# Performance work log

Hardware: AMD Instinct MI355X
Metric: run time of the kernel (lower is better)

## Reference

```python
import jax, jax.numpy as jnp
from jax import lax
import numpy as np

DIM = 768
NUM_TOKENS = 32
B, T, H, W = 16, 1, 32, 32


def setup_inputs() -> dict:
    key = jax.random.key(0)
    ks = jax.random.split(key, 10)
    return {
        "x": jax.random.normal(ks[0], (B, DIM, T, H, W), dtype=jnp.float32),
        "pos": jax.random.normal(ks[1], (B, DIM, T, H, W), dtype=jnp.float32),
        "bn_weight": jax.random.uniform(ks[2], (DIM,), dtype=jnp.float32, minval=0.5, maxval=1.5),
        "bn_bias": jax.random.normal(ks[3], (DIM,), dtype=jnp.float32) * 0.1,
        "bn_mean": jax.random.normal(ks[4], (DIM,), dtype=jnp.float32) * 0.1,
        "bn_var": jax.random.uniform(ks[5], (DIM,), dtype=jnp.float32, minval=0.5, maxval=1.5),
        "dw_weight": jax.random.normal(ks[6], (DIM, 1, 3, 3), dtype=jnp.float32) * 0.1,
        "dw_bias": jax.random.normal(ks[7], (DIM,), dtype=jnp.float32) * 0.1,
        "pw_weight": jax.random.normal(ks[8], (NUM_TOKENS, DIM, 1, 1), dtype=jnp.float32) * 0.05,
        "pw_bias": jax.random.normal(ks[9], (NUM_TOKENS,), dtype=jnp.float32) * 0.1,
    }


def _hardswish(x):
    return x * jnp.clip(x + 3.0, 0.0, 6.0) * (1.0 / 6.0)


def reference(x, pos, bn_weight, bn_bias, bn_mean, bn_var,
              dw_weight, dw_bias, pw_weight, pw_bias):
    eps = 1e-5
    f = x[:, :, 0]  # [B, C, H, W]
    # BatchNorm2d (inference form with running stats)
    scale = bn_weight * lax.rsqrt(bn_var + eps)          # [C]
    shift = bn_bias - bn_mean * scale                    # [C]
    f = f * scale[None, :, None, None] + shift[None, :, None, None]
    # depthwise 3x3 conv (groups = C)
    h = lax.conv_general_dilated(
        f, dw_weight, window_strides=(1, 1), padding="SAME",
        feature_group_count=DIM,
        dimension_numbers=("NCHW", "OIHW", "NCHW"))
    h = h + dw_bias[None, :, None, None]
    h = _hardswish(h)
    # pointwise 1x1 conv -> num_tokens channels
    s = lax.conv_general_dilated(
        h, pw_weight, window_strides=(1, 1), padding="SAME",
        dimension_numbers=("NCHW", "OIHW", "NCHW"))
    s = s + pw_bias[None, :, None, None]                 # [B, Nt, H, W]
    b, nt, hh, ww = s.shape
    st = s.reshape(b, nt, hh * ww)                       # [B, Nt, HW]
    # hard-argmax mask over spatial dim (ties -> multiple ones, as in torch)
    mask = (st == jnp.max(st, axis=2, keepdims=True)).astype(st.dtype)
    feat = f.reshape(b, DIM, hh * ww).transpose(0, 2, 1)  # [B, HW, C]
    result = mask @ feat                                  # [B, Nt, C]
    p = pos[:, :, 0].reshape(b, DIM, hh * ww).transpose(0, 2, 1)
    p = mask @ p                                          # [B, Nt, C]
    return result, p, mask
```

## Files before the change

kernel.cpp:

```cpp
#include <hip/hip_runtime.h>
#include <math.h>

#define DIMC 768
#define BATCH 16
#define HWSZ 1024
#define NT 32
#define SCH 16
#define CHPB 48

#define OUT_P_OFF    393216
#define OUT_MASK_OFF 786432

#define WS_WT_OFF 8388608

__global__ __launch_bounds__(256) void k0_transpose(
    const float* __restrict__ pww, float* __restrict__ wt)
{
    int i = blockIdx.x * 256 + threadIdx.x;
    wt[i] = pww[(i & 31) * DIMC + (i >> 5)];
}


#define ACC4(G) float a##G##0 = 0.f, a##G##1 = 0.f, a##G##2 = 0.f, a##G##3 = 0.f;
#define PW4(G, W) { a##G##0 = fmaf(hs, W.x, a##G##0); a##G##1 = fmaf(hs, W.y, a##G##1); \
                    a##G##2 = fmaf(hs, W.z, a##G##2); a##G##3 = fmaf(hs, W.w, a##G##3); }
#define STG4(G) { po[(size_t)(4*G+0) << 10] = a##G##0; po[(size_t)(4*G+1) << 10] = a##G##1; \
                  po[(size_t)(4*G+2) << 10] = a##G##2; po[(size_t)(4*G+3) << 10] = a##G##3; }

__global__ __launch_bounds__(256) void kf_fused(
    const float* __restrict__ x,
    const float* __restrict__ bnw, const float* __restrict__ bnb,
    const float* __restrict__ bnm, const float* __restrict__ bnv,
    const float* __restrict__ dww, const float* __restrict__ dwb,
    const float* __restrict__ wt,
    float* __restrict__ partials)
{
    const int b   = blockIdx.z;
    const int scc = blockIdx.y;
    const int cb0 = scc * CHPB;
    const int r0  = blockIdx.x * 8;
    const int tid = threadIdx.x;
    const int rl  = tid >> 5;
    const int col = tid & 31;

    __shared__ float st[2][340];
    float* S0 = &st[0][0];
    for (int i = tid; i < 680; i += 256) S0[i] = 0.0f;

    const int i1t = tid + 256;
    const int sr0 = tid / 34, sc0 = tid - sr0 * 34;
    const int sr1 = i1t / 34, sc1 = i1t - sr1 * 34;
    const int rr0 = r0 - 1 + sr0, cl0 = sc0 - 1;
    const int rr1 = r0 - 1 + sr1, cl1 = sc1 - 1;
    const bool valid0 = (rr0 >= 0 && rr0 < 32 && cl0 >= 0 && cl0 < 32);
    const bool valid1 = (i1t < 340) && (rr1 >= 0 && rr1 < 32 && cl1 >= 0 && cl1 < 32);
    const int off0 = rr0 * 32 + cl0;
    const int off1 = rr1 * 32 + cl1;

    const float* xb = x + (size_t)(b * DIMC) * HWSZ;

    {
        const int c = cb0;
        float scale = bnw[c] * rsqrtf(bnv[c] + 1e-5f);
        float shift = bnb[c] - bnm[c] * scale;
        const float* xc = xb + (size_t)c * HWSZ;
        if (valid0) st[0][tid] = xc[off0] * scale + shift;
        if (valid1) st[0][i1t] = xc[off1] * scale + shift;
    }
    __syncthreads();

    ACC4(0) ACC4(1) ACC4(2) ACC4(3) ACC4(4) ACC4(5) ACC4(6) ACC4(7)

    const int base = rl * 34 + col;

    for (int k = 0; k < CHPB; ++k) {
        const int c = cb0 + k;
        const float* S = st[k & 1];

        float g0 = 0.f, g1 = 0.f, scale = 0.f, shift = 0.f;
        if (k < CHPB - 1) {
            const int cn = c + 1;
            scale = bnw[cn] * rsqrtf(bnv[cn] + 1e-5f);
            shift = bnb[cn] - bnm[cn] * scale;
            const float* xc = xb + (size_t)cn * HWSZ;
            if (valid0) g0 = xc[off0];
            if (valid1) g1 = xc[off1];
        }

        const float* wd = dww + c * 9;
        float racc = dwb[c];
        racc = fmaf(wd[0], S[base +  0], racc);
        racc = fmaf(wd[1], S[base +  1], racc);
        racc = fmaf(wd[2], S[base +  2], racc);
        racc = fmaf(wd[3], S[base + 34], racc);
        racc = fmaf(wd[4], S[base + 35], racc);
        racc = fmaf(wd[5], S[base + 36], racc);
        racc = fmaf(wd[6], S[base + 68], racc);
        racc = fmaf(wd[7], S[base + 69], racc);
        racc = fmaf(wd[8], S[base + 70], racc);
        float clp = fminf(fmaxf(racc + 3.0f, 0.0f), 6.0f);
        float hs  = racc * clp * (1.0f / 6.0f);

        const float4* wv = (const float4*)(wt + c * NT);
        float4 wA = wv[0], wB = wv[1], wC = wv[2], wD = wv[3],
               wE = wv[4], wF = wv[5], wG = wv[6], wH = wv[7];
        PW4(0, wA) PW4(1, wB) PW4(2, wC) PW4(3, wD)
        PW4(4, wE) PW4(5, wF) PW4(6, wG) PW4(7, wH)

        if (k < CHPB - 1) {
            float* Sn = &st[(k & 1) ^ 1][0];
            if (valid0) Sn[tid] = fmaf(g0, scale, shift);
            if (valid1) Sn[i1t] = fmaf(g1, scale, shift);
        }
        __syncthreads();
    }

    float* po = partials + ((size_t)(scc * BATCH + b) * NT) * HWSZ
              + blockIdx.x * 256 + tid;
    STG4(0) STG4(1) STG4(2) STG4(3) STG4(4) STG4(5) STG4(6) STG4(7)
}

__global__ __launch_bounds__(256) void k3_mask_gather(
    const float* __restrict__ partials,
    const float* __restrict__ x, const float* __restrict__ posin,
    const float* __restrict__ bnw, const float* __restrict__ bnb,
    const float* __restrict__ bnm, const float* __restrict__ bnv,
    float* __restrict__ out)
{
    int bt = blockIdx.x;
    int b  = bt >> 5;
    int t  = bt & 31;
    int tid = threadIdx.x;

    const float* pp = partials + ((size_t)(b * NT) + t) * HWSZ;
    float v[4];
    float m = -INFINITY;
#pragma unroll
    for (int i = 0; i < 4; ++i) {
        int pos = tid + 256 * i;
        float acc = 0.0f;
#pragma unroll
        for (int s = 0; s < SCH; ++s)
            acc += pp[(size_t)s * (BATCH * NT * HWSZ) + pos];
        v[i] = acc;
        m = fmaxf(m, acc);
    }
#pragma unroll
    for (int off = 32; off; off >>= 1)
        m = fmaxf(m, __shfl_xor(m, off));
    __shared__ float wm[4];
    if ((tid & 63) == 0) wm[tid >> 6] = m;
    __syncthreads();
    m = fmaxf(fmaxf(wm[0], wm[1]), fmaxf(wm[2], wm[3]));

    __shared__ int nmatch;
    __shared__ int matchpos[16];
    if (tid == 0) nmatch = 0;
    __syncthreads();

    float* maskp = out + OUT_MASK_OFF + (size_t)bt * HWSZ;
#pragma unroll
    for (int i = 0; i < 4; ++i) {
        int pos = tid + 256 * i;
        int hit = (v[i] == m);
        maskp[pos] = hit ? 1.0f : 0.0f;
        if (hit) {
            int k = atomicAdd(&nmatch, 1);
            if (k < 16) matchpos[k] = pos;
        }
    }
    __syncthreads();
    int nm = nmatch < 16 ? nmatch : 16;

    const float* xb = x + (size_t)b * DIMC * HWSZ;
    const float* pb = posin + (size_t)b * DIMC * HWSZ;
    for (int c = tid; c < DIMC; c += 256) {
        float scale = bnw[c] * rsqrtf(bnv[c] + 1e-5f);
        float shift = bnb[c] - bnm[c] * scale;
        float rf = 0.0f, rp = 0.0f;
        for (int k = 0; k < nm; ++k) {
            int pos = matchpos[k];
            rf += xb[(size_t)c * HWSZ + pos] * scale + shift;
            rp += pb[(size_t)c * HWSZ + pos];
        }
        out[(size_t)bt * DIMC + c] = rf;
        out[OUT_P_OFF + (size_t)bt * DIMC + c] = rp;
    }
}

extern "C" void kernel_launch(void* const* d_in, const int* in_sizes, int n_in,
                              void* d_out, int out_size, void* d_ws, size_t ws_size,
                              hipStream_t stream)
{
    const float* x    = (const float*)d_in[0];
    const float* pos  = (const float*)d_in[1];
    const float* bnw  = (const float*)d_in[2];
    const float* bnb  = (const float*)d_in[3];
    const float* bnm  = (const float*)d_in[4];
    const float* bnv  = (const float*)d_in[5];
    const float* dww  = (const float*)d_in[6];
    const float* dwb  = (const float*)d_in[7];
    const float* pww  = (const float*)d_in[8];
    float* out = (float*)d_out;

    float* partials = (float*)d_ws;
    float* wt       = (float*)d_ws + WS_WT_OFF;

    k0_transpose<<<96, 256, 0, stream>>>(pww, wt);
    kf_fused<<<dim3(4, SCH, BATCH), 256, 0, stream>>>(x, bnw, bnb, bnm, bnv,
                                                      dww, dwb, wt, partials);
    k3_mask_gather<<<BATCH * NT, 256, 0, stream>>>(partials, x, pos,
                                                   bnw, bnb, bnm, bnv, out);
}
```

Before: 66.83 us.

## Stage four channels per barrier in fused conv and vectorize mask reduction

The fused depthwise+pointwise kernel now loads and normalizes four input channels per shared-memory stage instead of one. This cuts the number of __syncthreads from 48 to 12 per block and gives each thread more independent global loads in flight. The mask-gather kernel reads the split-K partials and writes the mask with float4 accesses instead of strided scalars. The cost is more shared memory and registers (six prefetch slots plus select logic), which may lower occupancy.

```diff
diff --git a/kernel.cpp b/kernel.cpp
--- a/kernel.cpp
+++ b/kernel.cpp
@@ -7,6 +7,8 @@
 #define NT 32
 #define SCH 16
 #define CHPB 48
+#define CPM 4
+#define NMAC 12
 
 #define OUT_P_OFF    393216
 #define OUT_MASK_OFF 786432
@@ -26,6 +28,35 @@
                     a##G##2 = fmaf(hs, W.z, a##G##2); a##G##3 = fmaf(hs, W.w, a##G##3); }
 #define STG4(G) { po[(size_t)(4*G+0) << 10] = a##G##0; po[(size_t)(4*G+1) << 10] = a##G##1; \
                   po[(size_t)(4*G+2) << 10] = a##G##2; po[(size_t)(4*G+3) << 10] = a##G##3; }
+
+#define CONV_PW(Q) { \
+    const int c = cm + Q; \
+    const float* wd = dww + c * 9; \
+    float r = dwb[c]; \
+    const float* S = Sc + (Q) * 340 + base; \
+    r = fmaf(wd[0], S[0],  r); \
+    r = fmaf(wd[1], S[1],  r); \
+    r = fmaf(wd[2], S[2],  r); \
+    r = fmaf(wd[3], S[34], r); \
+    r = fmaf(wd[4], S[35], r); \
+    r = fmaf(wd[5], S[36], r); \
+    r = fmaf(wd[6], S[68], r); \
+    r = fmaf(wd[7], S[69], r); \
+    r = fmaf(wd[8], S[70], r); \
+    float clp = fminf(fmaxf(r + 3.0f, 0.0f), 6.0f); \
+    float hs  = r * clp * (1.0f / 6.0f); \
+    const float4* wv = (const float4*)(wt + c * NT); \
+    float4 wA = wv[0], wB = wv[1], wC = wv[2], wD = wv[3], \
+           wE = wv[4], wF = wv[5], wG = wv[6], wH = wv[7]; \
+    PW4(0, wA) PW4(1, wB) PW4(2, wC) PW4(3, wD) \
+    PW4(4, wE) PW4(5, wF) PW4(6, wG) PW4(7, wH) }
+
+__device__ __forceinline__ float sel4(int cu, float v0, float v1, float v2, float v3)
+{
+    float a = (cu & 1) ? v1 : v0;
+    float b = (cu & 1) ? v3 : v2;
+    return (cu & 2) ? b : a;
+}
 
 __global__ __launch_bounds__(256) void kf_fused(
     const float* __restrict__ x,
@@ -43,29 +74,42 @@
     const int rl  = tid >> 5;
     const int col = tid & 31;
 
-    __shared__ float st[2][340];
-    float* S0 = &st[0][0];
-    for (int i = tid; i < 680; i += 256) S0[i] = 0.0f;
-
-    const int i1t = tid + 256;
-    const int sr0 = tid / 34, sc0 = tid - sr0 * 34;
-    const int sr1 = i1t / 34, sc1 = i1t - sr1 * 34;
-    const int rr0 = r0 - 1 + sr0, cl0 = sc0 - 1;
-    const int rr1 = r0 - 1 + sr1, cl1 = sc1 - 1;
-    const bool valid0 = (rr0 >= 0 && rr0 < 32 && cl0 >= 0 && cl0 < 32);
-    const bool valid1 = (i1t < 340) && (rr1 >= 0 && rr1 < 32 && cl1 >= 0 && cl1 < 32);
-    const int off0 = rr0 * 32 + cl0;
-    const int off1 = rr1 * 32 + cl1;
+    __shared__ float st[2][CPM * 340];
+
+    for (int i = tid; i < 2 * CPM * 340; i += 256) ((float*)st)[i] = 0.0f;
+
+    int  soff[6]; bool svalid[6]; int scu[6];
+#pragma unroll
+    for (int u = 0; u < 6; ++u) {
+        int idx = tid + 256 * u;
+        int cu  = idx / 340;
+        int rem = idx - cu * 340;
+        int sr  = rem / 34, sc = rem - sr * 34;
+        int rr  = r0 - 1 + sr, cc = sc - 1;
+        svalid[u] = (idx < CPM * 340) && rr >= 0 && rr < 32 && cc >= 0 && cc < 32;
+        scu[u]  = cu;
+        soff[u] = cu * HWSZ + rr * 32 + cc;
+    }
 
     const float* xb = x + (size_t)(b * DIMC) * HWSZ;
 
     {
-        const int c = cb0;
-        float scale = bnw[c] * rsqrtf(bnv[c] + 1e-5f);
-        float shift = bnb[c] - bnm[c] * scale;
-        const float* xc = xb + (size_t)c * HWSZ;
-        if (valid0) st[0][tid] = xc[off0] * scale + shift;
-        if (valid1) st[0][i1t] = xc[off1] * scale + shift;
+        const int cm = cb0;
+        float g[6];
+#pragma unroll
+        for (int u = 0; u < 6; ++u)
+            g[u] = svalid[u] ? xb[(size_t)cm * HWSZ + soff[u]] : 0.0f;
+        float s0 = bnw[cm+0] * rsqrtf(bnv[cm+0] + 1e-5f), h0 = bnb[cm+0] - bnm[cm+0] * s0;
+        float s1 = bnw[cm+1] * rsqrtf(bnv[cm+1] + 1e-5f), h1 = bnb[cm+1] - bnm[cm+1] * s1;
+        float s2 = bnw[cm+2] * rsqrtf(bnv[cm+2] + 1e-5f), h2 = bnb[cm+2] - bnm[cm+2] * s2;
+        float s3 = bnw[cm+3] * rsqrtf(bnv[cm+3] + 1e-5f), h3 = bnb[cm+3] - bnm[cm+3] * s3;
+        float* Sn = &st[0][0];
+#pragma unroll
+        for (int u = 0; u < 6; ++u) {
+            float scl = sel4(scu[u], s0, s1, s2, s3);
+            float shf = sel4(scu[u], h0, h1, h2, h3);
+            if (svalid[u]) Sn[tid + 256 * u] = fmaf(g[u], scl, shf);
+        }
     }
     __syncthreads();
 
@@ -73,44 +117,33 @@
 
     const int base = rl * 34 + col;
 
-    for (int k = 0; k < CHPB; ++k) {
-        const int c = cb0 + k;
-        const float* S = st[k & 1];
-
-        float g0 = 0.f, g1 = 0.f, scale = 0.f, shift = 0.f;
-        if (k < CHPB - 1) {
-            const int cn = c + 1;
-            scale = bnw[cn] * rsqrtf(bnv[cn] + 1e-5f);
-            shift = bnb[cn] - bnm[cn] * scale;
-            const float* xc = xb + (size_t)cn * HWSZ;
-            if (valid0) g0 = xc[off0];
-            if (valid1) g1 = xc[off1];
-        }
-
-        const float* wd = dww + c * 9;
-        float racc = dwb[c];
-        racc = fmaf(wd[0], S[base +  0], racc);
-        racc = fmaf(wd[1], S[base +  1], racc);
-        racc = fmaf(wd[2], S[base +  2], racc);
-        racc = fmaf(wd[3], S[base + 34], racc);
-        racc = fmaf(wd[4], S[base + 35], racc);
-        racc = fmaf(wd[5], S[base + 36], racc);
-        racc = fmaf(wd[6], S[base + 68], racc);
-        racc = fmaf(wd[7], S[base + 69], racc);
-        racc = fmaf(wd[8], S[base + 70], racc);
-        float clp = fminf(fmaxf(racc + 3.0f, 0.0f), 6.0f);
-        float hs  = racc * clp * (1.0f / 6.0f);
-
-        const float4* wv = (const float4*)(wt + c * NT);
-        float4 wA = wv[0], wB = wv[1], wC = wv[2], wD = wv[3],
-               wE = wv[4], wF = wv[5], wG = wv[6], wH = wv[7];
-        PW4(0, wA) PW4(1, wB) PW4(2, wC) PW4(3, wD)
-        PW4(4, wE) PW4(5, wF) PW4(6, wG) PW4(7, wH)
-
-        if (k < CHPB - 1) {
-            float* Sn = &st[(k & 1) ^ 1][0];
-            if (valid0) Sn[tid] = fmaf(g0, scale, shift);
-            if (valid1) Sn[i1t] = fmaf(g1, scale, shift);
+    for (int m = 0; m < NMAC; ++m) {
+        const int cm = cb0 + m * CPM;
+        const float* Sc = &st[m & 1][0];
+
+        float g[6];
+        if (m < NMAC - 1) {
+            const int cn = cm + CPM;
+#pragma unroll
+            for (int u = 0; u < 6; ++u)
+                g[u] = svalid[u] ? xb[(size_t)cn * HWSZ + soff[u]] : 0.0f;
+        }
+
+        CONV_PW(0) CONV_PW(1) CONV_PW(2) CONV_PW(3)
+
+        if (m < NMAC - 1) {
+            const int cn = cm + CPM;
+            float s0 = bnw[cn+0] * rsqrtf(bnv[cn+0] + 1e-5f), h0 = bnb[cn+0] - bnm[cn+0] * s0;
+            float s1 = bnw[cn+1] * rsqrtf(bnv[cn+1] + 1e-5f), h1 = bnb[cn+1] - bnm[cn+1] * s1;
+            float s2 = bnw[cn+2] * rsqrtf(bnv[cn+2] + 1e-5f), h2 = bnb[cn+2] - bnm[cn+2] * s2;
+            float s3 = bnw[cn+3] * rsqrtf(bnv[cn+3] + 1e-5f), h3 = bnb[cn+3] - bnm[cn+3] * s3;
+            float* Sn = &st[(m & 1) ^ 1][0];
+#pragma unroll
+            for (int u = 0; u < 6; ++u) {
+                float scl = sel4(scu[u], s0, s1, s2, s3);
+                float shf = sel4(scu[u], h0, h1, h2, h3);
+                if (svalid[u]) Sn[tid + 256 * u] = fmaf(g[u], scl, shf);
+            }
         }
         __syncthreads();
     }
@@ -132,19 +165,15 @@
     int t  = bt & 31;
     int tid = threadIdx.x;
 
-    const float* pp = partials + ((size_t)(b * NT) + t) * HWSZ;
-    float v[4];
-    float m = -INFINITY;
-#pragma unroll
-    for (int i = 0; i < 4; ++i) {
-        int pos = tid + 256 * i;
-        float acc = 0.0f;
-#pragma unroll
-        for (int s = 0; s < SCH; ++s)
-            acc += pp[(size_t)s * (BATCH * NT * HWSZ) + pos];
-        v[i] = acc;
-        m = fmaxf(m, acc);
-    }
+    const float4* pp4 = (const float4*)(partials + ((size_t)(b * NT) + t) * HWSZ) + tid;
+    float4 acc = make_float4(0.f, 0.f, 0.f, 0.f);
+#pragma unroll
+    for (int s = 0; s < SCH; ++s) {
+        float4 u = pp4[(size_t)s * (BATCH * NT * HWSZ / 4)];
+        acc.x += u.x; acc.y += u.y; acc.z += u.z; acc.w += u.w;
+    }
+
+    float m = fmaxf(fmaxf(acc.x, acc.y), fmaxf(acc.z, acc.w));
 #pragma unroll
     for (int off = 32; off; off >>= 1)
         m = fmaxf(m, __shfl_xor(m, off));
@@ -159,16 +188,19 @@
     __syncthreads();
 
     float* maskp = out + OUT_MASK_OFF + (size_t)bt * HWSZ;
-#pragma unroll
-    for (int i = 0; i < 4; ++i) {
-        int pos = tid + 256 * i;
-        int hit = (v[i] == m);
-        maskp[pos] = hit ? 1.0f : 0.0f;
+    float4 mask4;
+    const float* av = &acc.x;
+    float* mv = &mask4.x;
+#pragma unroll
+    for (int j = 0; j < 4; ++j) {
+        int hit = (av[j] == m);
+        mv[j] = hit ? 1.0f : 0.0f;
         if (hit) {
             int k = atomicAdd(&nmatch, 1);
-            if (k < 16) matchpos[k] = pos;
-        }
-    }
+            if (k < 16) matchpos[k] = 4 * tid + j;
+        }
+    }
+    ((float4*)maskp)[tid] = mask4;
     __syncthreads();
     int nm = nmatch < 16 ? nmatch : 16;
 
```

Result: slower. 87.79 us (+31.4%).

## Split token accumulators across 512 threads and prepack per-channel params

Applied to the files above, without the earlier changes.

The fused depthwise+pointwise kernel now runs 512 threads per block. Each half of the block accumulates 16 of the 32 tokens, which lowers register pressure per thread but duplicates the depthwise conv work across the two halves. A prep kernel packs the depthwise weights, bias and BN scale/shift into 12-float records per channel, and the main loop software-prefetches these and the next channel's pointwise weights as vectors. The mask/gather kernel now reads partials and writes the mask with float4 accesses.

```diff
diff --git a/kernel.cpp b/kernel.cpp
--- a/kernel.cpp
+++ b/kernel.cpp
@@ -12,112 +12,128 @@
 #define OUT_MASK_OFF 786432
 
 #define WS_WT_OFF 8388608
-
-__global__ __launch_bounds__(256) void k0_transpose(
-    const float* __restrict__ pww, float* __restrict__ wt)
-{
-    int i = blockIdx.x * 256 + threadIdx.x;
-    wt[i] = pww[(i & 31) * DIMC + (i >> 5)];
-}
-
-
-#define ACC4(G) float a##G##0 = 0.f, a##G##1 = 0.f, a##G##2 = 0.f, a##G##3 = 0.f;
-#define PW4(G, W) { a##G##0 = fmaf(hs, W.x, a##G##0); a##G##1 = fmaf(hs, W.y, a##G##1); \
-                    a##G##2 = fmaf(hs, W.z, a##G##2); a##G##3 = fmaf(hs, W.w, a##G##3); }
-#define STG4(G) { po[(size_t)(4*G+0) << 10] = a##G##0; po[(size_t)(4*G+1) << 10] = a##G##1; \
-                  po[(size_t)(4*G+2) << 10] = a##G##2; po[(size_t)(4*G+3) << 10] = a##G##3; }
-
-__global__ __launch_bounds__(256) void kf_fused(
-    const float* __restrict__ x,
+#define WS_PK_OFF 8413184
+
+typedef float v4f __attribute__((ext_vector_type(4)));
+
+__global__ __launch_bounds__(256) void k0_prep(
+    const float* __restrict__ pww,
+    const float* __restrict__ dww, const float* __restrict__ dwb,
     const float* __restrict__ bnw, const float* __restrict__ bnb,
     const float* __restrict__ bnm, const float* __restrict__ bnv,
-    const float* __restrict__ dww, const float* __restrict__ dwb,
-    const float* __restrict__ wt,
+    float* __restrict__ wt, float* __restrict__ pk)
+{
+    int i = blockIdx.x * 256 + threadIdx.x;
+    if (blockIdx.x < 96) {
+        wt[i] = pww[(i & 31) * DIMC + (i >> 5)];
+    } else {
+        int c = i - 24576;
+        if (c < DIMC) {
+            float* o = pk + c * 12;
+#pragma unroll
+            for (int j = 0; j < 9; ++j) o[j] = dww[c * 9 + j];
+            o[9] = dwb[c];
+            float scale = bnw[c] * rsqrtf(bnv[c] + 1e-5f);
+            o[10] = scale;
+            o[11] = bnb[c] - bnm[c] * scale;
+        }
+    }
+}
+
+__global__ __launch_bounds__(512) void kf_fused(
+    const float* __restrict__ x,
+    const float* __restrict__ wt, const float* __restrict__ pk,
     float* __restrict__ partials)
 {
-    const int b   = blockIdx.z;
-    const int scc = blockIdx.y;
-    const int cb0 = scc * CHPB;
-    const int r0  = blockIdx.x * 8;
-    const int tid = threadIdx.x;
-    const int rl  = tid >> 5;
-    const int col = tid & 31;
+    const int b    = blockIdx.z;
+    const int scc  = blockIdx.y;
+    const int cb0  = scc * CHPB;
+    const int r0   = blockIdx.x * 8;
+    const int tid  = threadIdx.x;
+    const int pos  = tid & 255;
+    const int rl   = pos >> 5;
+    const int col  = pos & 31;
+    const int tok0 = (tid >> 8) << 4;
 
     __shared__ float st[2][340];
-    float* S0 = &st[0][0];
-    for (int i = tid; i < 680; i += 256) S0[i] = 0.0f;
-
-    const int i1t = tid + 256;
-    const int sr0 = tid / 34, sc0 = tid - sr0 * 34;
-    const int sr1 = i1t / 34, sc1 = i1t - sr1 * 34;
-    const int rr0 = r0 - 1 + sr0, cl0 = sc0 - 1;
-    const int rr1 = r0 - 1 + sr1, cl1 = sc1 - 1;
-    const bool valid0 = (rr0 >= 0 && rr0 < 32 && cl0 >= 0 && cl0 < 32);
-    const bool valid1 = (i1t < 340) && (rr1 >= 0 && rr1 < 32 && cl1 >= 0 && cl1 < 32);
-    const int off0 = rr0 * 32 + cl0;
-    const int off1 = rr1 * 32 + cl1;
-
-    const float* xb = x + (size_t)(b * DIMC) * HWSZ;
-
+    for (int i = tid; i < 680; i += 512) ((float*)st)[i] = 0.0f;
+
+    const int sr = tid / 34, sc = tid - sr * 34;
+    const int rr = r0 - 1 + sr, cc = sc - 1;
+    const bool sval = (tid < 340) && rr >= 0 && rr < 32 && cc >= 0 && cc < 32;
+    const int  soff = rr * 32 + cc;
+
+    const float* xb  = x  + (size_t)(b * DIMC + cb0) * HWSZ;
+    const float* pkb = pk + (size_t)cb0 * 12;
+    const float* wtb = wt + (size_t)cb0 * NT + tok0;
+
+    v4f P0 = *(const v4f*)(pkb + 0);
+    v4f P1 = *(const v4f*)(pkb + 4);
+    v4f P2 = *(const v4f*)(pkb + 8);
+    v4f W0 = *(const v4f*)(wtb + 0);
+    v4f W1 = *(const v4f*)(wtb + 4);
+    v4f W2 = *(const v4f*)(wtb + 8);
+    v4f W3 = *(const v4f*)(wtb + 12);
     {
-        const int c = cb0;
-        float scale = bnw[c] * rsqrtf(bnv[c] + 1e-5f);
-        float shift = bnb[c] - bnm[c] * scale;
-        const float* xc = xb + (size_t)c * HWSZ;
-        if (valid0) st[0][tid] = xc[off0] * scale + shift;
-        if (valid1) st[0][i1t] = xc[off1] * scale + shift;
-    }
-    __syncthreads();
-
-    ACC4(0) ACC4(1) ACC4(2) ACC4(3) ACC4(4) ACC4(5) ACC4(6) ACC4(7)
-
+        float g = sval ? xb[soff] : 0.0f;
+        if (sval) st[0][tid] = fmaf(g, P2.z, P2.w);
+    }
+    __syncthreads();
+
+    v4f A0 = {0,0,0,0}, A1 = {0,0,0,0}, A2 = {0,0,0,0}, A3 = {0,0,0,0};
     const int base = rl * 34 + col;
 
     for (int k = 0; k < CHPB; ++k) {
-        const int c = cb0 + k;
-        const float* S = st[k & 1];
-
-        float g0 = 0.f, g1 = 0.f, scale = 0.f, shift = 0.f;
+        const float* S = &st[k & 1][0];
+
+        float g = 0.0f;
+        v4f NP0, NP1, NP2, N0, N1, N2, N3;
         if (k < CHPB - 1) {
-            const int cn = c + 1;
-            scale = bnw[cn] * rsqrtf(bnv[cn] + 1e-5f);
-            shift = bnb[cn] - bnm[cn] * scale;
-            const float* xc = xb + (size_t)cn * HWSZ;
-            if (valid0) g0 = xc[off0];
-            if (valid1) g1 = xc[off1];
-        }
-
-        const float* wd = dww + c * 9;
-        float racc = dwb[c];
-        racc = fmaf(wd[0], S[base +  0], racc);
-        racc = fmaf(wd[1], S[base +  1], racc);
-        racc = fmaf(wd[2], S[base +  2], racc);
-        racc = fmaf(wd[3], S[base + 34], racc);
-        racc = fmaf(wd[4], S[base + 35], racc);
-        racc = fmaf(wd[5], S[base + 36], racc);
-        racc = fmaf(wd[6], S[base + 68], racc);
-        racc = fmaf(wd[7], S[base + 69], racc);
-        racc = fmaf(wd[8], S[base + 70], racc);
-        float clp = fminf(fmaxf(racc + 3.0f, 0.0f), 6.0f);
-        float hs  = racc * clp * (1.0f / 6.0f);
-
-        const float4* wv = (const float4*)(wt + c * NT);
-        float4 wA = wv[0], wB = wv[1], wC = wv[2], wD = wv[3],
-               wE = wv[4], wF = wv[5], wG = wv[6], wH = wv[7];
-        PW4(0, wA) PW4(1, wB) PW4(2, wC) PW4(3, wD)
-        PW4(4, wE) PW4(5, wF) PW4(6, wG) PW4(7, wH)
+            const float* pn = pkb + (k + 1) * 12;
+            NP0 = *(const v4f*)(pn + 0);
+            NP1 = *(const v4f*)(pn + 4);
+            NP2 = *(const v4f*)(pn + 8);
+            const float* wn = wtb + (k + 1) * NT;
+            N0 = *(const v4f*)(wn + 0);
+            N1 = *(const v4f*)(wn + 4);
+            N2 = *(const v4f*)(wn + 8);
+            N3 = *(const v4f*)(wn + 12);
+            if (sval) g = xb[(size_t)(k + 1) * HWSZ + soff];
+        }
+
+        float r = P2.y;
+        r = fmaf(P0.x, S[base +  0], r);
+        r = fmaf(P0.y, S[base +  1], r);
+        r = fmaf(P0.z, S[base +  2], r);
+        r = fmaf(P0.w, S[base + 34], r);
+        r = fmaf(P1.x, S[base + 35], r);
+        r = fmaf(P1.y, S[base + 36], r);
+        r = fmaf(P1.z, S[base + 68], r);
+        r = fmaf(P1.w, S[base + 69], r);
+        r = fmaf(P2.x, S[base + 70], r);
+        float clp = fminf(fmaxf(r + 3.0f, 0.0f), 6.0f);
+        float hs  = r * clp * (1.0f / 6.0f);
+
+        v4f hsv = {hs, hs, hs, hs};
+        A0 = __builtin_elementwise_fma(hsv, W0, A0);
+        A1 = __builtin_elementwise_fma(hsv, W1, A1);
+        A2 = __builtin_elementwise_fma(hsv, W2, A2);
+        A3 = __builtin_elementwise_fma(hsv, W3, A3);
 
         if (k < CHPB - 1) {
-            float* Sn = &st[(k & 1) ^ 1][0];
-            if (valid0) Sn[tid] = fmaf(g0, scale, shift);
-            if (valid1) Sn[i1t] = fmaf(g1, scale, shift);
+            if (sval) st[(k & 1) ^ 1][tid] = fmaf(g, NP2.z, NP2.w);
+            P0 = NP0; P1 = NP1; P2 = NP2;
+            W0 = N0;  W1 = N1;  W2 = N2;  W3 = N3;
         }
         __syncthreads();
     }
 
-    float* po = partials + ((size_t)(scc * BATCH + b) * NT) * HWSZ
-              + blockIdx.x * 256 + tid;
-    STG4(0) STG4(1) STG4(2) STG4(3) STG4(4) STG4(5) STG4(6) STG4(7)
+    float* po = partials + (((size_t)(scc * BATCH + b)) * NT + tok0) * HWSZ
+              + blockIdx.x * 256 + pos;
+    po[ 0 << 10] = A0.x; po[ 1 << 10] = A0.y; po[ 2 << 10] = A0.z; po[ 3 << 10] = A0.w;
+    po[ 4 << 10] = A1.x; po[ 5 << 10] = A1.y; po[ 6 << 10] = A1.z; po[ 7 << 10] = A1.w;
+    po[ 8 << 10] = A2.x; po[ 9 << 10] = A2.y; po[10 << 10] = A2.z; po[11 << 10] = A2.w;
+    po[12 << 10] = A3.x; po[13 << 10] = A3.y; po[14 << 10] = A3.z; po[15 << 10] = A3.w;
 }
 
 __global__ __launch_bounds__(256) void k3_mask_gather(
@@ -132,19 +148,15 @@
     int t  = bt & 31;
     int tid = threadIdx.x;
 
-    const float* pp = partials + ((size_t)(b * NT) + t) * HWSZ;
-    float v[4];
-    float m = -INFINITY;
-#pragma unroll
-    for (int i = 0; i < 4; ++i) {
-        int pos = tid + 256 * i;
-        float acc = 0.0f;
-#pragma unroll
-        for (int s = 0; s < SCH; ++s)
-            acc += pp[(size_t)s * (BATCH * NT * HWSZ) + pos];
-        v[i] = acc;
-        m = fmaxf(m, acc);
-    }
+    const float4* pp4 = (const float4*)(partials + ((size_t)(b * NT) + t) * HWSZ) + tid;
+    float4 acc = make_float4(0.f, 0.f, 0.f, 0.f);
+#pragma unroll
+    for (int s = 0; s < SCH; ++s) {
+        float4 u = pp4[(size_t)s * (BATCH * NT * HWSZ / 4)];
+        acc.x += u.x; acc.y += u.y; acc.z += u.z; acc.w += u.w;
+    }
+
+    float m = fmaxf(fmaxf(acc.x, acc.y), fmaxf(acc.z, acc.w));
 #pragma unroll
     for (int off = 32; off; off >>= 1)
         m = fmaxf(m, __shfl_xor(m, off));
@@ -159,16 +171,19 @@
     __syncthreads();
 
     float* maskp = out + OUT_MASK_OFF + (size_t)bt * HWSZ;
-#pragma unroll
-    for (int i = 0; i < 4; ++i) {
-        int pos = tid + 256 * i;
-        int hit = (v[i] == m);
-        maskp[pos] = hit ? 1.0f : 0.0f;
+    float4 mask4;
+    const float* av = &acc.x;
+    float* mv = &mask4.x;
+#pragma unroll
+    for (int j = 0; j < 4; ++j) {
+        int hit = (av[j] == m);
+        mv[j] = hit ? 1.0f : 0.0f;
         if (hit) {
             int k = atomicAdd(&nmatch, 1);
-            if (k < 16) matchpos[k] = pos;
-        }
-    }
+            if (k < 16) matchpos[k] = 4 * tid + j;
+        }
+    }
+    ((float4*)maskp)[tid] = mask4;
     __syncthreads();
     int nm = nmatch < 16 ? nmatch : 16;
 
@@ -205,10 +220,10 @@
 
     float* partials = (float*)d_ws;
     float* wt       = (float*)d_ws + WS_WT_OFF;
-
-    k0_transpose<<<96, 256, 0, stream>>>(pww, wt);
-    kf_fused<<<dim3(4, SCH, BATCH), 256, 0, stream>>>(x, bnw, bnb, bnm, bnv,
-                                                      dww, dwb, wt, partials);
+    float* pk       = (float*)d_ws + WS_PK_OFF;
+
+    k0_prep<<<99, 256, 0, stream>>>(pww, dww, dwb, bnw, bnb, bnm, bnv, wt, pk);
+    kf_fused<<<dim3(4, SCH, BATCH), 512, 0, stream>>>(x, wt, pk, partials);
     k3_mask_gather<<<BATCH * NT, 256, 0, stream>>>(partials, x, pos,
                                                    bnw, bnb, bnm, bnv, out);
 }
```

Result: slower. 100.2 us (+50.0%).
